# Kernel tuning notes

Measured on AMD Instinct MI355X. Metric: run time of the kernel, lower is better.

Reference implementation:

```python
import jax, jax.numpy as jnp
import numpy as np

N_NODES = 8192
F_DIM = 64
A_DIM = 8
HID = 32
AVG_DEG = 16.0


def _linear_params(key, fan_in, fan_out):
    # torch nn.Linear default init: U(-1/sqrt(fan_in), 1/sqrt(fan_in))
    s = 1.0 / np.sqrt(fan_in)
    k1, k2 = jax.random.split(key)
    W = jax.random.uniform(k1, (fan_in, fan_out), minval=-s, maxval=s, dtype=jnp.float32)
    b = jax.random.uniform(k2, (fan_out,), minval=-s, maxval=s, dtype=jnp.float32)
    return W, b


def setup_inputs() -> dict:
    key = jax.random.key(0)
    ks = jax.random.split(key, 12)
    N, Fd, Ad, H = N_NODES, F_DIM, A_DIM, HID

    features = jax.random.normal(ks[0], (N, Fd), dtype=jnp.float32)
    # sparse symmetric binary adjacency, zero diagonal (edge weights are discarded
    # by the original code -> all edges weight 1, so binary is the faithful form)
    u = jax.random.uniform(ks[1], (N, N), dtype=jnp.float32)
    adj = (u < AVG_DEG / N).astype(jnp.float32)
    adj = jnp.maximum(adj, adj.T) * (1.0 - jnp.eye(N, dtype=jnp.float32))
    mask = jax.random.uniform(ks[2], (N,), dtype=jnp.float32)  # RL_indice (unused)
    action = jax.random.normal(ks[3], (N, Ad), dtype=jnp.float32)

    We1, be1 = _linear_params(ks[4], Fd + Ad, H)
    We2, be2 = _linear_params(ks[5], H, H)
    Wg, bg = _linear_params(ks[6], H, H)      # GCNConv weight + bias
    Wgd, bgd = _linear_params(ks[7], H, H)    # GraphConv_Dense
    Wp1, bp1 = _linear_params(ks[8], 2 * H, H)
    Wp2, bp2 = _linear_params(ks[9], H, H)
    Wv, bv = _linear_params(ks[10], H, 1)

    return dict(features=features, adjacency=adjacency_fix(adj), mask=mask, action=action,
                We1=We1, be1=be1, We2=We2, be2=be2, Wg=Wg, bg=bg, Wgd=Wgd, bgd=bgd,
                Wp1=Wp1, bp1=bp1, Wp2=Wp2, bp2=bp2, Wv=Wv, bv=bv)


def adjacency_fix(adj):
    return adj


def reference(features, adjacency, mask, action,
              We1, be1, We2, be2, Wg, bg, Wgd, bgd,
              Wp1, bp1, Wp2, bp2, Wv, bv):
    # encoder
    X = jax.nn.relu(jnp.concatenate([features, action], axis=1) @ We1 + be1)  # [N,32]
    X = jax.nn.relu(X @ We2 + be2)                                            # [N,32]

    # GCNConv: out = D^{-1/2} (A + I) D^{-1/2} (X W) + b   (self-loops added, deg incl. self)
    deg = jnp.sum(adjacency, axis=1) + 1.0                 # [N]
    dinv = jax.lax.rsqrt(deg)                              # [N]
    S = (X @ Wg) * dinv[:, None]                           # [N,32] scaled messages
    Xg = (adjacency @ S + S) * dinv[:, None] + bg          # aggregate (A@S) + self-loop (S)
    Xg = jax.nn.relu(Xg)
    Xg = jax.nn.relu(Xg @ Wgd + bgd)

    # policy/value head on [graph || encoder] features
    P = jnp.concatenate([Xg, X], axis=1)                   # [N,64]
    P = jax.nn.relu(P @ Wp1 + bp1)
    P = jax.nn.relu(P @ Wp2 + bp2)
    V = P @ Wv + bv                                        # [N,1]
    return V
```

## Files before the change

### kernel.cpp

```cpp
#include <hip/hip_runtime.h>
#include <math.h>

#define NN 8192
#define FD 64
#define AD 8
#define H  32
#define CAP 128
#define NENC (NN / 256)

typedef unsigned short u16;

#define OW1 0
#define OW2 2304
#define OWG 3328
#define OB1 4352
#define OB2 4384
#define SMEM_FLOATS 4416

__global__ __launch_bounds__(256) void pre_k(const float4* __restrict__ adj,
                                             const float* __restrict__ feat,
                                             const float* __restrict__ act,
                                             const float* __restrict__ We1,
                                             const float* __restrict__ be1,
                                             const float* __restrict__ We2,
                                             const float* __restrict__ be2,
                                             const float* __restrict__ Wg,
                                             u16* __restrict__ nbr,
                                             int* __restrict__ cnt,
                                             float* __restrict__ dinv,
                                             float* __restrict__ X,
                                             float* __restrict__ T) {
    __shared__ float smem[SMEM_FLOATS];

    if (blockIdx.x >= NENC) {
        int* s_cnt = (int*)smem;
        const int row = blockIdx.x - NENC;
        const float4* arow = adj + (size_t)row * (NN / 4);
        if (threadIdx.x == 0) *s_cnt = 0;
        __syncthreads();

        float4 v[8];
#pragma unroll
        for (int it = 0; it < 8; ++it) v[it] = arow[it * 256 + threadIdx.x];

        u16* myn = nbr + (size_t)row * CAP;
#pragma unroll
        for (int it = 0; it < 8; ++it) {
            const int base = (it * 256 + threadIdx.x) * 4;
            const int nz0 = (v[it].x != 0.0f), nz1 = (v[it].y != 0.0f);
            const int nz2 = (v[it].z != 0.0f), nz3 = (v[it].w != 0.0f);
            const int local = nz0 + nz1 + nz2 + nz3;
            if (local) {
                int slot = atomicAdd(s_cnt, local);
                if (slot + local <= CAP) {
                    if (nz0) myn[slot++] = (u16)(base);
                    if (nz1) myn[slot++] = (u16)(base + 1);
                    if (nz2) myn[slot++] = (u16)(base + 2);
                    if (nz3) myn[slot++] = (u16)(base + 3);
                }
            }
        }
        __syncthreads();
        if (threadIdx.x == 0) {
            const int c = *s_cnt;
            cnt[row]  = (c < CAP) ? c : CAP;
            dinv[row] = 1.0f / sqrtf((float)c + 1.0f);
        }
    } else {
        for (int i = threadIdx.x; i < (FD + AD) * H; i += 256) smem[OW1 + i] = We1[i];
        for (int i = threadIdx.x; i < H * H; i += 256) {
            smem[OW2 + i] = We2[i];
            smem[OWG + i] = Wg[i];
        }
        if (threadIdx.x < H) {
            smem[OB1 + threadIdx.x] = be1[threadIdx.x];
            smem[OB2 + threadIdx.x] = be2[threadIdx.x];
        }
        __syncthreads();

        const int row = blockIdx.x * 256 + threadIdx.x;

        float in[FD + AD];
        const float4* f4 = (const float4*)(feat + (size_t)row * FD);
#pragma unroll
        for (int i = 0; i < FD / 4; ++i) {
            float4 v = f4[i];
            in[4 * i] = v.x; in[4 * i + 1] = v.y; in[4 * i + 2] = v.z; in[4 * i + 3] = v.w;
        }
        const float4* a4 = (const float4*)(act + (size_t)row * AD);
#pragma unroll
        for (int i = 0; i < AD / 4; ++i) {
            float4 v = a4[i];
            in[FD + 4 * i] = v.x; in[FD + 4 * i + 1] = v.y;
            in[FD + 4 * i + 2] = v.z; in[FD + 4 * i + 3] = v.w;
        }

        float h1[H];
#pragma unroll
        for (int o = 0; o < H; ++o) h1[o] = smem[OB1 + o];
#pragma unroll
        for (int i = 0; i < FD + AD; ++i) {
            const float xi = in[i];
#pragma unroll
            for (int o = 0; o < H; ++o) h1[o] = fmaf(xi, smem[OW1 + i * H + o], h1[o]);
        }
#pragma unroll
        for (int o = 0; o < H; ++o) h1[o] = fmaxf(h1[o], 0.0f);

        float h2[H];
#pragma unroll
        for (int o = 0; o < H; ++o) h2[o] = smem[OB2 + o];
#pragma unroll
        for (int i = 0; i < H; ++i) {
            const float xi = h1[i];
#pragma unroll
            for (int o = 0; o < H; ++o) h2[o] = fmaf(xi, smem[OW2 + i * H + o], h2[o]);
        }
#pragma unroll
        for (int o = 0; o < H; ++o) h2[o] = fmaxf(h2[o], 0.0f);

        float* Xr = X + (size_t)row * H;
#pragma unroll
        for (int o = 0; o < H; o += 4)
            *(float4*)(Xr + o) = make_float4(h2[o], h2[o + 1], h2[o + 2], h2[o + 3]);

        float t[H];
#pragma unroll
        for (int o = 0; o < H; ++o) t[o] = 0.0f;
#pragma unroll
        for (int i = 0; i < H; ++i) {
            const float xi = h2[i];
#pragma unroll
            for (int o = 0; o < H; ++o) t[o] = fmaf(xi, smem[OWG + i * H + o], t[o]);
        }
        float* Tr = T + (size_t)row * H;
#pragma unroll
        for (int o = 0; o < H; o += 4)
            *(float4*)(Tr + o) = make_float4(t[o], t[o + 1], t[o + 2], t[o + 3]);
    }
}

__global__ __launch_bounds__(64) void fin_k(const float* __restrict__ T,
                                            const float* __restrict__ X,
                                            const u16* __restrict__ nbr,
                                            const int* __restrict__ cnt,
                                            const float* __restrict__ dinv,
                                            const float* __restrict__ bg,
                                            const float* __restrict__ Wgd,
                                            const float* __restrict__ bgd,
                                            const float* __restrict__ Wp1,
                                            const float* __restrict__ bp1,
                                            const float* __restrict__ Wp2,
                                            const float* __restrict__ bp2,
                                            const float* __restrict__ Wv,
                                            const float* __restrict__ bv,
                                            float* __restrict__ out) {
    __shared__ float sbg[H];
    __shared__ float sWgd[H * H];
    __shared__ float sbgd[H];
    __shared__ float sWp1[2 * H * H];
    __shared__ float sbp1[H];
    __shared__ float sWp2[H * H];
    __shared__ float sbp2[H];
    __shared__ float sWv[H];
    __shared__ float sbv;
    for (int i = threadIdx.x; i < H * H; i += 64) { sWgd[i] = Wgd[i]; sWp2[i] = Wp2[i]; }
    for (int i = threadIdx.x; i < 2 * H * H; i += 64) sWp1[i] = Wp1[i];
    if (threadIdx.x < H) {
        sbg[threadIdx.x]  = bg[threadIdx.x];
        sbgd[threadIdx.x] = bgd[threadIdx.x];
        sbp1[threadIdx.x] = bp1[threadIdx.x];
        sbp2[threadIdx.x] = bp2[threadIdx.x];
        sWv[threadIdx.x]  = Wv[threadIdx.x];
    }
    if (threadIdx.x == 0) sbv = bv[0];
    __syncthreads();

    const int row = blockIdx.x * 64 + threadIdx.x;
    const float di = dinv[row];

    float acc[H];
    const float4* Tr = (const float4*)(T + (size_t)row * H);
#pragma unroll
    for (int q = 0; q < H / 4; ++q) {
        float4 v = Tr[q];
        acc[4 * q]     = v.x * di; acc[4 * q + 1] = v.y * di;
        acc[4 * q + 2] = v.z * di; acc[4 * q + 3] = v.w * di;
    }

    const int n = cnt[row];
    const u16* myn = nbr + (size_t)row * CAP;
    int e = 0;
    for (; e + 4 <= n; e += 4) {
        const ushort4 ii = *(const ushort4*)(myn + e);
        const int j0 = ii.x, j1 = ii.y, j2 = ii.z, j3 = ii.w;
        const float d0 = dinv[j0], d1 = dinv[j1], d2 = dinv[j2], d3 = dinv[j3];
        const float4* T0 = (const float4*)(T + (size_t)j0 * H);
        const float4* T1 = (const float4*)(T + (size_t)j1 * H);
        const float4* T2 = (const float4*)(T + (size_t)j2 * H);
        const float4* T3 = (const float4*)(T + (size_t)j3 * H);
#pragma unroll
        for (int q = 0; q < H / 4; ++q) {
            const float4 a = T0[q], b = T1[q], c = T2[q], d = T3[q];
            acc[4 * q]     = fmaf(a.x, d0, acc[4 * q]);
            acc[4 * q + 1] = fmaf(a.y, d0, acc[4 * q + 1]);
            acc[4 * q + 2] = fmaf(a.z, d0, acc[4 * q + 2]);
            acc[4 * q + 3] = fmaf(a.w, d0, acc[4 * q + 3]);
            acc[4 * q]     = fmaf(b.x, d1, acc[4 * q]);
            acc[4 * q + 1] = fmaf(b.y, d1, acc[4 * q + 1]);
            acc[4 * q + 2] = fmaf(b.z, d1, acc[4 * q + 2]);
            acc[4 * q + 3] = fmaf(b.w, d1, acc[4 * q + 3]);
            acc[4 * q]     = fmaf(c.x, d2, acc[4 * q]);
            acc[4 * q + 1] = fmaf(c.y, d2, acc[4 * q + 1]);
            acc[4 * q + 2] = fmaf(c.z, d2, acc[4 * q + 2]);
            acc[4 * q + 3] = fmaf(c.w, d2, acc[4 * q + 3]);
            acc[4 * q]     = fmaf(d.x, d3, acc[4 * q]);
            acc[4 * q + 1] = fmaf(d.y, d3, acc[4 * q + 1]);
            acc[4 * q + 2] = fmaf(d.z, d3, acc[4 * q + 2]);
            acc[4 * q + 3] = fmaf(d.w, d3, acc[4 * q + 3]);
        }
    }
    for (; e < n; ++e) {
        const int j = myn[e];
        const float dj = dinv[j];
        const float4* Tj = (const float4*)(T + (size_t)j * H);
#pragma unroll
        for (int q = 0; q < H / 4; ++q) {
            const float4 v = Tj[q];
            acc[4 * q]     = fmaf(v.x, dj, acc[4 * q]);
            acc[4 * q + 1] = fmaf(v.y, dj, acc[4 * q + 1]);
            acc[4 * q + 2] = fmaf(v.z, dj, acc[4 * q + 2]);
            acc[4 * q + 3] = fmaf(v.w, dj, acc[4 * q + 3]);
        }
    }

    float xg[H];
#pragma unroll
    for (int k = 0; k < H; ++k) xg[k] = fmaxf(fmaf(acc[k], di, sbg[k]), 0.0f);

    float xg2[H];
#pragma unroll
    for (int o = 0; o < H; ++o) xg2[o] = sbgd[o];
#pragma unroll
    for (int k = 0; k < H; ++k) {
        const float xk = xg[k];
#pragma unroll
        for (int o = 0; o < H; ++o) xg2[o] = fmaf(xk, sWgd[k * H + o], xg2[o]);
    }
#pragma unroll
    for (int o = 0; o < H; ++o) xg2[o] = fmaxf(xg2[o], 0.0f);

    float x[H];
    const float4* Xr = (const float4*)(X + (size_t)row * H);
#pragma unroll
    for (int q = 0; q < H / 4; ++q) {
        float4 v = Xr[q];
        x[4 * q] = v.x; x[4 * q + 1] = v.y; x[4 * q + 2] = v.z; x[4 * q + 3] = v.w;
    }

    float p1[H];
#pragma unroll
    for (int o = 0; o < H; ++o) p1[o] = sbp1[o];
#pragma unroll
    for (int k = 0; k < H; ++k) {
        const float xk = xg2[k];
#pragma unroll
        for (int o = 0; o < H; ++o) p1[o] = fmaf(xk, sWp1[k * H + o], p1[o]);
    }
#pragma unroll
    for (int k = 0; k < H; ++k) {
        const float xk = x[k];
#pragma unroll
        for (int o = 0; o < H; ++o) p1[o] = fmaf(xk, sWp1[(H + k) * H + o], p1[o]);
    }
#pragma unroll
    for (int o = 0; o < H; ++o) p1[o] = fmaxf(p1[o], 0.0f);

    float p2[H];
#pragma unroll
    for (int o = 0; o < H; ++o) p2[o] = sbp2[o];
#pragma unroll
    for (int k = 0; k < H; ++k) {
        const float xk = p1[k];
#pragma unroll
        for (int o = 0; o < H; ++o) p2[o] = fmaf(xk, sWp2[k * H + o], p2[o]);
    }

    float v = sbv;
#pragma unroll
    for (int k = 0; k < H; ++k) v = fmaf(fmaxf(p2[k], 0.0f), sWv[k], v);

    out[row] = v;
}

extern "C" void kernel_launch(void* const* d_in, const int* in_sizes, int n_in,
                              void* d_out, int out_size, void* d_ws, size_t ws_size,
                              hipStream_t stream) {
    (void)in_sizes; (void)n_in; (void)out_size; (void)ws_size;

    const float* feat = (const float*)d_in[0];
    const float* adj  = (const float*)d_in[1];
    const float* act  = (const float*)d_in[3];
    const float* We1  = (const float*)d_in[4];
    const float* be1  = (const float*)d_in[5];
    const float* We2  = (const float*)d_in[6];
    const float* be2  = (const float*)d_in[7];
    const float* Wg   = (const float*)d_in[8];
    const float* bg   = (const float*)d_in[9];
    const float* Wgd  = (const float*)d_in[10];
    const float* bgd  = (const float*)d_in[11];
    const float* Wp1  = (const float*)d_in[12];
    const float* bp1  = (const float*)d_in[13];
    const float* Wp2  = (const float*)d_in[14];
    const float* bp2  = (const float*)d_in[15];
    const float* Wv   = (const float*)d_in[16];
    const float* bv   = (const float*)d_in[17];

    char* ws = (char*)d_ws;
    u16*   nbr  = (u16*)ws;
    char*  p    = ws + (size_t)NN * CAP * sizeof(u16);
    int*   cnt  = (int*)p;            p += (size_t)NN * 4;
    float* dinv = (float*)p;          p += (size_t)NN * 4;
    float* X    = (float*)p;          p += (size_t)NN * H * 4;
    float* T    = (float*)p;

    float* out = (float*)d_out;

    pre_k<<<NENC + NN, 256, 0, stream>>>((const float4*)adj, feat, act,
                                         We1, be1, We2, be2, Wg,
                                         nbr, cnt, dinv, X, T);
    fin_k<<<NN / 64, 64, 0, stream>>>(T, X, nbr, cnt, dinv, bg, Wgd, bgd,
                                      Wp1, bp1, Wp2, bp2, Wv, bv, out);
}
```

Baseline: 423.9 us.

## Scan only the upper triangle of the symmetric adjacency and mirror edges with atomics

The neighbor-list build now reads only entries above the diagonal of each adjacency row. Each edge it finds is inserted into both endpoints' lists through global atomics on a zeroed count array. Rows p and N-1-p are paired per block to balance the triangular work. This roughly halves the dominant dense-adjacency read, but it relies on the adjacency being symmetric and adds global atomic traffic. The stored dinv array is also removed and recomputed from counts in the gather kernel, and the encoder input loop is reorganised to consume float4 loads directly.

```diff
diff --git a/kernel.cpp b/kernel.cpp
--- a/kernel.cpp
+++ b/kernel.cpp
@@ -7,6 +7,7 @@
 #define H  32
 #define CAP 128
 #define NENC (NN / 256)
+#define NPAIR (NN / 2)
 
 typedef unsigned short u16;
 
@@ -17,55 +18,70 @@
 #define OB2 4384
 #define SMEM_FLOATS 4416
 
-__global__ __launch_bounds__(256) void pre_k(const float4* __restrict__ adj,
-                                             const float* __restrict__ feat,
-                                             const float* __restrict__ act,
-                                             const float* __restrict__ We1,
-                                             const float* __restrict__ be1,
-                                             const float* __restrict__ We2,
-                                             const float* __restrict__ be2,
-                                             const float* __restrict__ Wg,
-                                             u16* __restrict__ nbr,
-                                             int* __restrict__ cnt,
-                                             float* __restrict__ dinv,
-                                             float* __restrict__ X,
-                                             float* __restrict__ T) {
+__device__ __forceinline__ void scan_row(const float4* __restrict__ arow, const int r,
+                                         int* __restrict__ cnt, u16* __restrict__ nbr) {
+    int i4 = ((r + 1) >> 2) + (int)threadIdx.x;
+    if (i4 >= NN / 4) return;
+    float4 v = arow[i4];
+    for (;;) {
+        const int nx = i4 + 256;
+        const bool more = (nx < NN / 4);
+        float4 vn;
+        if (more) vn = arow[nx];
+
+        const int base = i4 * 4;
+        if (v.x != 0.0f && base > r) {
+            const int s = atomicAdd(&cnt[r], 1);
+            if (s < CAP) nbr[(size_t)r * CAP + s] = (u16)base;
+            const int s2 = atomicAdd(&cnt[base], 1);
+            if (s2 < CAP) nbr[(size_t)base * CAP + s2] = (u16)r;
+        }
+        if (v.y != 0.0f && base + 1 > r) {
+            const int c = base + 1;
+            const int s = atomicAdd(&cnt[r], 1);
+            if (s < CAP) nbr[(size_t)r * CAP + s] = (u16)c;
+            const int s2 = atomicAdd(&cnt[c], 1);
+            if (s2 < CAP) nbr[(size_t)c * CAP + s2] = (u16)r;
+        }
+        if (v.z != 0.0f && base + 2 > r) {
+            const int c = base + 2;
+            const int s = atomicAdd(&cnt[r], 1);
+            if (s < CAP) nbr[(size_t)r * CAP + s] = (u16)c;
+            const int s2 = atomicAdd(&cnt[c], 1);
+            if (s2 < CAP) nbr[(size_t)c * CAP + s2] = (u16)r;
+        }
+        if (v.w != 0.0f && base + 3 > r) {
+            const int c = base + 3;
+            const int s = atomicAdd(&cnt[r], 1);
+            if (s < CAP) nbr[(size_t)r * CAP + s] = (u16)c;
+            const int s2 = atomicAdd(&cnt[c], 1);
+            if (s2 < CAP) nbr[(size_t)c * CAP + s2] = (u16)r;
+        }
+
+        if (!more) break;
+        v = vn; i4 = nx;
+    }
+}
+
+__global__ __launch_bounds__(256, 8) void pre_k(const float4* __restrict__ adj,
+                                                const float* __restrict__ feat,
+                                                const float* __restrict__ act,
+                                                const float* __restrict__ We1,
+                                                const float* __restrict__ be1,
+                                                const float* __restrict__ We2,
+                                                const float* __restrict__ be2,
+                                                const float* __restrict__ Wg,
+                                                u16* __restrict__ nbr,
+                                                int* __restrict__ cnt,
+                                                float* __restrict__ X,
+                                                float* __restrict__ T) {
     __shared__ float smem[SMEM_FLOATS];
 
     if (blockIdx.x >= NENC) {
-        int* s_cnt = (int*)smem;
-        const int row = blockIdx.x - NENC;
-        const float4* arow = adj + (size_t)row * (NN / 4);
-        if (threadIdx.x == 0) *s_cnt = 0;
-        __syncthreads();
-
-        float4 v[8];
-#pragma unroll
-        for (int it = 0; it < 8; ++it) v[it] = arow[it * 256 + threadIdx.x];
-
-        u16* myn = nbr + (size_t)row * CAP;
-#pragma unroll
-        for (int it = 0; it < 8; ++it) {
-            const int base = (it * 256 + threadIdx.x) * 4;
-            const int nz0 = (v[it].x != 0.0f), nz1 = (v[it].y != 0.0f);
-            const int nz2 = (v[it].z != 0.0f), nz3 = (v[it].w != 0.0f);
-            const int local = nz0 + nz1 + nz2 + nz3;
-            if (local) {
-                int slot = atomicAdd(s_cnt, local);
-                if (slot + local <= CAP) {
-                    if (nz0) myn[slot++] = (u16)(base);
-                    if (nz1) myn[slot++] = (u16)(base + 1);
-                    if (nz2) myn[slot++] = (u16)(base + 2);
-                    if (nz3) myn[slot++] = (u16)(base + 3);
-                }
-            }
-        }
-        __syncthreads();
-        if (threadIdx.x == 0) {
-            const int c = *s_cnt;
-            cnt[row]  = (c < CAP) ? c : CAP;
-            dinv[row] = 1.0f / sqrtf((float)c + 1.0f);
-        }
+        const int p = blockIdx.x - NENC;
+        scan_row(adj + (size_t)p * (NN / 4), p, cnt, nbr);
+        const int r2 = NN - 1 - p;
+        scan_row(adj + (size_t)r2 * (NN / 4), r2, cnt, nbr);
     } else {
         for (int i = threadIdx.x; i < (FD + AD) * H; i += 256) smem[OW1 + i] = We1[i];
         for (int i = threadIdx.x; i < H * H; i += 256) {
@@ -80,29 +96,37 @@
 
         const int row = blockIdx.x * 256 + threadIdx.x;
 
-        float in[FD + AD];
+        float h1[H];
+#pragma unroll
+        for (int o = 0; o < H; ++o) h1[o] = smem[OB1 + o];
+
         const float4* f4 = (const float4*)(feat + (size_t)row * FD);
 #pragma unroll
         for (int i = 0; i < FD / 4; ++i) {
-            float4 v = f4[i];
-            in[4 * i] = v.x; in[4 * i + 1] = v.y; in[4 * i + 2] = v.z; in[4 * i + 3] = v.w;
+            const float4 v = f4[i];
+            const int b = 4 * i;
+#pragma unroll
+            for (int o = 0; o < H; ++o) h1[o] = fmaf(v.x, smem[OW1 + (b + 0) * H + o], h1[o]);
+#pragma unroll
+            for (int o = 0; o < H; ++o) h1[o] = fmaf(v.y, smem[OW1 + (b + 1) * H + o], h1[o]);
+#pragma unroll
+            for (int o = 0; o < H; ++o) h1[o] = fmaf(v.z, smem[OW1 + (b + 2) * H + o], h1[o]);
+#pragma unroll
+            for (int o = 0; o < H; ++o) h1[o] = fmaf(v.w, smem[OW1 + (b + 3) * H + o], h1[o]);
         }
         const float4* a4 = (const float4*)(act + (size_t)row * AD);
 #pragma unroll
         for (int i = 0; i < AD / 4; ++i) {
-            float4 v = a4[i];
-            in[FD + 4 * i] = v.x; in[FD + 4 * i + 1] = v.y;
-            in[FD + 4 * i + 2] = v.z; in[FD + 4 * i + 3] = v.w;
-        }
-
-        float h1[H];
-#pragma unroll
-        for (int o = 0; o < H; ++o) h1[o] = smem[OB1 + o];
-#pragma unroll
-        for (int i = 0; i < FD + AD; ++i) {
-            const float xi = in[i];
-#pragma unroll
-            for (int o = 0; o < H; ++o) h1[o] = fmaf(xi, smem[OW1 + i * H + o], h1[o]);
+            const float4 v = a4[i];
+            const int b = FD + 4 * i;
+#pragma unroll
+            for (int o = 0; o < H; ++o) h1[o] = fmaf(v.x, smem[OW1 + (b + 0) * H + o], h1[o]);
+#pragma unroll
+            for (int o = 0; o < H; ++o) h1[o] = fmaf(v.y, smem[OW1 + (b + 1) * H + o], h1[o]);
+#pragma unroll
+            for (int o = 0; o < H; ++o) h1[o] = fmaf(v.z, smem[OW1 + (b + 2) * H + o], h1[o]);
+#pragma unroll
+            for (int o = 0; o < H; ++o) h1[o] = fmaf(v.w, smem[OW1 + (b + 3) * H + o], h1[o]);
         }
 #pragma unroll
         for (int o = 0; o < H; ++o) h1[o] = fmaxf(h1[o], 0.0f);
@@ -124,19 +148,18 @@
         for (int o = 0; o < H; o += 4)
             *(float4*)(Xr + o) = make_float4(h2[o], h2[o + 1], h2[o + 2], h2[o + 3]);
 
-        float t[H];
-#pragma unroll
-        for (int o = 0; o < H; ++o) t[o] = 0.0f;
+#pragma unroll
+        for (int o = 0; o < H; ++o) h1[o] = 0.0f;
 #pragma unroll
         for (int i = 0; i < H; ++i) {
             const float xi = h2[i];
 #pragma unroll
-            for (int o = 0; o < H; ++o) t[o] = fmaf(xi, smem[OWG + i * H + o], t[o]);
+            for (int o = 0; o < H; ++o) h1[o] = fmaf(xi, smem[OWG + i * H + o], h1[o]);
         }
         float* Tr = T + (size_t)row * H;
 #pragma unroll
         for (int o = 0; o < H; o += 4)
-            *(float4*)(Tr + o) = make_float4(t[o], t[o + 1], t[o + 2], t[o + 3]);
+            *(float4*)(Tr + o) = make_float4(h1[o], h1[o + 1], h1[o + 2], h1[o + 3]);
     }
 }
 
@@ -144,7 +167,6 @@
                                             const float* __restrict__ X,
                                             const u16* __restrict__ nbr,
                                             const int* __restrict__ cnt,
-                                            const float* __restrict__ dinv,
                                             const float* __restrict__ bg,
                                             const float* __restrict__ Wgd,
                                             const float* __restrict__ bgd,
@@ -177,7 +199,9 @@
     __syncthreads();
 
     const int row = blockIdx.x * 64 + threadIdx.x;
-    const float di = dinv[row];
+    const int n_raw = cnt[row];
+    const int n = (n_raw < CAP) ? n_raw : CAP;
+    const float di = 1.0f / sqrtf((float)n_raw + 1.0f);
 
     float acc[H];
     const float4* Tr = (const float4*)(T + (size_t)row * H);
@@ -188,13 +212,16 @@
         acc[4 * q + 2] = v.z * di; acc[4 * q + 3] = v.w * di;
     }
 
-    const int n = cnt[row];
     const u16* myn = nbr + (size_t)row * CAP;
     int e = 0;
     for (; e + 4 <= n; e += 4) {
         const ushort4 ii = *(const ushort4*)(myn + e);
         const int j0 = ii.x, j1 = ii.y, j2 = ii.z, j3 = ii.w;
-        const float d0 = dinv[j0], d1 = dinv[j1], d2 = dinv[j2], d3 = dinv[j3];
+        const int c0 = cnt[j0], c1 = cnt[j1], c2 = cnt[j2], c3 = cnt[j3];
+        const float d0 = 1.0f / sqrtf((float)c0 + 1.0f);
+        const float d1 = 1.0f / sqrtf((float)c1 + 1.0f);
+        const float d2 = 1.0f / sqrtf((float)c2 + 1.0f);
+        const float d3 = 1.0f / sqrtf((float)c3 + 1.0f);
         const float4* T0 = (const float4*)(T + (size_t)j0 * H);
         const float4* T1 = (const float4*)(T + (size_t)j1 * H);
         const float4* T2 = (const float4*)(T + (size_t)j2 * H);
@@ -222,7 +249,8 @@
     }
     for (; e < n; ++e) {
         const int j = myn[e];
-        const float dj = dinv[j];
+        const int cj = cnt[j];
+        const float dj = 1.0f / sqrtf((float)cj + 1.0f);
         const float4* Tj = (const float4*)(T + (size_t)j * H);
 #pragma unroll
         for (int q = 0; q < H / 4; ++q) {
@@ -320,15 +348,15 @@
     u16*   nbr  = (u16*)ws;
     char*  p    = ws + (size_t)NN * CAP * sizeof(u16);
     int*   cnt  = (int*)p;            p += (size_t)NN * 4;
-    float* dinv = (float*)p;          p += (size_t)NN * 4;
     float* X    = (float*)p;          p += (size_t)NN * H * 4;
     float* T    = (float*)p;
 
     float* out = (float*)d_out;
 
-    pre_k<<<NENC + NN, 256, 0, stream>>>((const float4*)adj, feat, act,
-                                         We1, be1, We2, be2, Wg,
-                                         nbr, cnt, dinv, X, T);
-    fin_k<<<NN / 64, 64, 0, stream>>>(T, X, nbr, cnt, dinv, bg, Wgd, bgd,
+    hipMemsetAsync(cnt, 0, (size_t)NN * sizeof(int), stream);
+    pre_k<<<NENC + NPAIR, 256, 0, stream>>>((const float4*)adj, feat, act,
+                                            We1, be1, We2, be2, Wg,
+                                            nbr, cnt, X, T);
+    fin_k<<<NN / 64, 64, 0, stream>>>(T, X, nbr, cnt, bg, Wgd, bgd,
                                       Wp1, bp1, Wp2, bp2, Wv, bv, out);
 }
```

Result: no change. 431.6 us (+1.8%).
